# Kernel optimization log

Hardware: AMD Instinct MI355X
Metric: run time of the kernel (lower is better)

## Reference

```python
import jax, jax.numpy as jnp
import numpy as np
from functools import partial

B, N, T_HIST, T_FCST, HID, F, DEG = 16, 2000, 24, 24, 64, 8, 32
E_TOTAL = B * N * DEG


def setup_inputs() -> dict:
    key = jax.random.key(0)
    ks = jax.random.split(key, 20)
    s = 1.0 / np.sqrt(HID)
    # block-diagonal batched edge_index, as built by _process_adj_mat
    src = jax.random.randint(ks[0], (B, N * DEG), 0, N, dtype=jnp.int32)
    dst = jax.random.randint(ks[1], (B, N * DEG), 0, N, dtype=jnp.int32)
    off = (jnp.arange(B, dtype=jnp.int32) * N)[:, None]
    edge_index = jnp.stack([(src + off).reshape(-1), (dst + off).reshape(-1)], axis=0)
    return {
        "pm25_hist": jax.random.normal(ks[2], (B, T_HIST, N, 1), jnp.float32),
        "feature": jax.random.normal(ks[3], (B, T_HIST + T_FCST, N, F), jnp.float32),
        "edge_index": edge_index,
        "w_ih_enc": jax.random.normal(ks[4], (3 * HID, 2), jnp.float32) * s,
        "w_hh_enc": jax.random.normal(ks[5], (3 * HID, HID), jnp.float32) * s,
        "b_ih_enc": jnp.zeros((3 * HID,), jnp.float32),
        "b_hh_enc": jnp.zeros((3 * HID,), jnp.float32),
        "fc_w": jax.random.normal(ks[6], (1, HID), jnp.float32) * s,
        "fc_b": jnp.zeros((1,), jnp.float32),
        "cheb_w0": jax.random.normal(ks[7], (F + 1, 1), jnp.float32) * s,
        "cheb_w1": jax.random.normal(ks[8], (F + 1, 1), jnp.float32) * s,
        "cheb_b": jnp.zeros((1,), jnp.float32),
        "w_ih_dec": jax.random.normal(ks[9], (3 * HID, F + 2), jnp.float32) * s,
        "w_hh_dec": jax.random.normal(ks[10], (3 * HID, HID), jnp.float32) * s,
        "b_ih_dec": jnp.zeros((3 * HID,), jnp.float32),
        "b_hh_dec": jnp.zeros((3 * HID,), jnp.float32),
        "out_w": jax.random.normal(ks[11], (1, 2 * HID), jnp.float32) * s,
        "out_b": jnp.zeros((1,), jnp.float32),
    }


def gru(x, h, w_ih, w_hh, b_ih, b_hh):
    gi = x @ w_ih.T + b_ih
    gh = h @ w_hh.T + b_hh
    i_r, i_z, i_n = jnp.split(gi, 3, axis=-1)
    h_r, h_z, h_n = jnp.split(gh, 3, axis=-1)
    r = jax.nn.sigmoid(i_r + h_r)
    z = jax.nn.sigmoid(i_z + h_z)
    n = jnp.tanh(i_n + r * h_n)
    return (1.0 - z) * n + z * h


def cheb_conv(x, edge_index, w0, w1, b):
    # ChebConv K=2, sym norm, lambda_max=2 -> T1(L_hat) = -D^-1/2 A D^-1/2
    src, dst = edge_index[0], edge_index[1]
    ones = jnp.ones(src.shape, x.dtype)
    deg = jax.ops.segment_sum(ones, dst, num_segments=B * N)
    dis = jnp.where(deg > 0, jax.lax.rsqrt(jnp.maximum(deg, 1.0)), 0.0)
    norm = -(dis[src] * dis[dst])
    tx1 = jax.ops.segment_sum(norm[:, None] * x[src], dst, num_segments=B * N)
    return x @ w0 + tx1 @ w1 + b


def reference(pm25_hist, feature, edge_index, w_ih_enc, w_hh_enc, b_ih_enc, b_hh_enc,
              fc_w, fc_b, cheb_w0, cheb_w1, cheb_b, w_ih_dec, w_hh_dec, b_ih_dec,
              b_hh_dec, out_w, out_b):
    # ---------------- encoder ----------------
    h0 = jnp.zeros((B * N, HID), pm25_hist.dtype)
    x0 = jnp.zeros((B, N, 1), pm25_hist.dtype)

    def enc_step(carry, pm_t):
        hn, xn = carry
        x = jnp.concatenate([xn, pm_t], axis=-1).reshape(B * N, 2)
        hn = gru(x, hn, w_ih_enc, w_hh_enc, b_ih_enc, b_hh_enc)
        h3 = hn.reshape(B, N, HID)
        xn = h3 @ fc_w.T + fc_b
        return (hn, xn), h3

    (hn, xn), Hs = jax.lax.scan(enc_step, (h0, x0), pm25_hist.transpose(1, 0, 2, 3))
    H = Hs.transpose(1, 0, 2, 3)  # (B, T_HIST, N, HID)

    # ---------------- decoder ----------------
    def dec_step(carry, feat_t):
        hn, xn = carry
        x = jnp.concatenate([xn, feat_t], axis=-1)  # (B, N, F+1)
        xg = jax.nn.sigmoid(cheb_conv(x.reshape(B * N, F + 1), edge_index,
                                      cheb_w0, cheb_w1, cheb_b))
        x2 = jnp.concatenate([x, xg.reshape(B, N, 1)], axis=-1).reshape(B * N, F + 2)
        hn = gru(x2, hn, w_ih_dec, w_hh_dec, b_ih_dec, b_hh_dec)
        xn3 = hn.reshape(B, N, HID)
        energy = jnp.einsum('btnd,bnd->bnt', H, xn3)  # history attention
        alpha = jax.nn.softmax(energy, axis=2)
        a = jnp.einsum('bnt,btnd->bnd', alpha, H)
        xn = jnp.concatenate([a, xn3], axis=-1) @ out_w.T + out_b
        return (hn, xn), xn

    feats = feature[:, T_HIST:].transpose(1, 0, 2, 3)  # (T_FCST, B, N, F)
    _, preds = jax.lax.scan(dec_step, (hn, xn), feats)
    return preds.transpose(1, 0, 2, 3)  # (B, T_FCST, N, 1)
```

## Files before the change

### kernel.cpp

```cpp
#include <hip/hip_runtime.h>
#include <hip/hip_bf16.h>
#include <cstddef>
#include <cstdint>

constexpr int NB    = 16;
constexpr int NN    = 2000;
constexpr int TH    = 24;
constexpr int TF    = 24;
constexpr int HID   = 64;
constexpr int NF    = 8;
constexpr int NODES = NB * NN;
constexpr int ETOT  = NODES * 32;
constexpr int TT    = TH + TF;
constexpr int EBLK  = 32;
constexpr int NEBLK = NODES / EBLK;
constexpr int DBLK  = 64;
constexpr int NDBLK = NODES / DBLK;

typedef __attribute__((ext_vector_type(8))) short bf16x8;
typedef __attribute__((ext_vector_type(4))) float f32x4;
typedef uint16_t u16;

__device__ __forceinline__ float sigmoidf_(float x) { return 1.f / (1.f + __expf(-x)); }
__device__ __forceinline__ float tanhf_(float x) {
    float e = __expf(2.f * x);
    return 1.f - 2.f / (e + 1.f);
}
__device__ __forceinline__ u16 bfh(float x) {
    __hip_bfloat16 b = __float2bfloat16(x);
    u16 u; __builtin_memcpy(&u, &b, 2); return u;
}
__device__ __forceinline__ float bff(u16 u) { return __uint_as_float(((uint32_t)u) << 16); }
__device__ __forceinline__ uint32_t pk(u16 a, u16 b) { return (uint32_t)a | ((uint32_t)b << 16); }

__global__ void k_init(float* __restrict__ dis) {
    int i = blockIdx.x * blockDim.x + threadIdx.x;
    if (i < NODES) dis[i] = 0.f;
}

__global__ void k_deg(const int* __restrict__ ei, float* __restrict__ deg) {
    int e = blockIdx.x * blockDim.x + threadIdx.x;
    if (e < ETOT) atomicAdd(&deg[ei[ETOT + e]], 1.0f);
}

__global__ __launch_bounds__(256) void k_scan(const float* __restrict__ degf,
                                              int* __restrict__ row0,
                                              int* __restrict__ cnt)
{
    __shared__ int part[256];
    const int tid = threadIdx.x;
    const int per = NODES / 256;
    const int base = tid * per;
    int s = 0;
    for (int i = 0; i < per; i++) s += (int)degf[base + i];
    part[tid] = s;
    __syncthreads();
    for (int off = 1; off < 256; off <<= 1) {
        int v = (tid >= off) ? part[tid - off] : 0;
        __syncthreads();
        part[tid] += v;
        __syncthreads();
    }
    int run = (tid == 0) ? 0 : part[tid - 1];
    for (int i = 0; i < per; i++) {
        row0[base + i] = run;
        cnt[base + i]  = 0;
        run += (int)degf[base + i];
    }
    if (tid == 255) row0[NODES] = run;
}

__global__ void k_dis(float* __restrict__ dis) {
    int i = blockIdx.x * blockDim.x + threadIdx.x;
    if (i < NODES) {
        float d = dis[i];
        dis[i] = (d > 0.f) ? rsqrtf(fmaxf(d, 1.f)) : 0.f;
    }
}

__global__ void k_fill(const int* __restrict__ ei, const float* __restrict__ dis,
                       const int* __restrict__ row0, int* __restrict__ cnt,
                       int2* __restrict__ edge8)
{
    int e = blockIdx.x * blockDim.x + threadIdx.x;
    if (e < ETOT) {
        int s = ei[e];
        int d = ei[ETOT + e];
        float nv = -(dis[s] * dis[d]);
        int p = atomicAdd(&cnt[d], 1);
        edge8[row0[d] + p] = make_int2(s, __float_as_int(nv));
    }
}

__global__ void k_prepE(const float* __restrict__ whe, const float* __restrict__ fcw,
                        u16* __restrict__ AH, u16* __restrict__ AL)
{
    int i = blockIdx.x * blockDim.x + threadIdx.x;
    if (i < 208 * 64) {
        int r = i >> 6, k = i & 63;
        float v = (r < 192) ? whe[r * 64 + k] : ((r == 192) ? fcw[k] : 0.f);
        u16 hi = bfh(v);
        AH[i] = hi;
        AL[i] = bfh(v - bff(hi));
    }
}

__global__ void k_prepD(const float* __restrict__ whd, const float* __restrict__ wihd,
                        u16* __restrict__ AH, u16* __restrict__ AL)
{
    int i = blockIdx.x * blockDim.x + threadIdx.x;
    if (i < 256 * 96) {
        int r = i / 96, k = i - r * 96;
        float v = 0.f;
        if (k < 64) {
            if (r < 192) v = whd[r * 64 + k];
        } else if (k < 74) {
            int xi = k - 64;
            if (r < 128)       v = wihd[r * 10 + xi];
            else if (r >= 192) v = wihd[(r - 64) * 10 + xi];
        }
        u16 hi = bfh(v);
        AH[i] = hi;
        AL[i] = bfh(v - bff(hi));
    }
}

__global__ __launch_bounds__(256, 2) void k_encM(
    const float* __restrict__ pm, const u16* __restrict__ AeH, const u16* __restrict__ AeL,
    const float* __restrict__ w_ih, const float* __restrict__ b_ih, const float* __restrict__ b_hh,
    const float* __restrict__ fc_b, const float* __restrict__ feat, const float* __restrict__ cw1,
    u16* __restrict__ BgH, u16* __restrict__ BgL, u16* __restrict__ Hb,
    float* __restrict__ xn_buf, float* __restrict__ y1)
{
    __shared__ u16 BH[2][EBLK * 64], BL[2][EBLK * 64];
    __shared__ float pmL[TH * EBLK];
    __shared__ float xnL[EBLK];

    const int tid = threadIdx.x;
    const int l   = tid & 63;
    const int wv  = __builtin_amdgcn_readfirstlane(tid >> 6);
    const int n0  = blockIdx.x * EBLK;
    const int cn  = l & 15;
    const int kg  = l >> 4;
    const int c0  = wv * 16 + kg * 4;

    for (int i = tid; i < EBLK * 64 / 2; i += 256) {
        ((uint32_t*)BH[0])[i] = 0u;
        ((uint32_t*)BL[0])[i] = 0u;
    }
    for (int i = tid; i < TH * EBLK; i += 256) {
        int t = i >> 5, n = i & 31;
        int node = n0 + n, b = node / NN, nn2 = node - b * NN;
        pmL[i] = pm[(b * TH + t) * NN + nn2];
    }
    bf16x8 AHf[4][2], ALf[4][2];
    #pragma unroll
    for (int s = 0; s < 4; s++) {
        #pragma unroll
        for (int ks = 0; ks < 2; ks++) {
            bf16x8 zh = {0,0,0,0,0,0,0,0};
            AHf[s][ks] = zh; ALf[s][ks] = zh;
            if (s < 3 || wv == 0) {
                int row = (wv + 4 * s) * 16 + cn;
                int off = row * 64 + ks * 32 + kg * 8;
                AHf[s][ks] = *(const bf16x8*)(AeH + off);
                ALf[s][ks] = *(const bf16x8*)(AeL + off);
            }
        }
    }
    float bR[4], bZ[4], biN[4], bhN[4];
    float wR0[4], wR1[4], wZ0[4], wZ1[4], wN0[4], wN1[4];
    #pragma unroll
    for (int j = 0; j < 4; j++) {
        int c = c0 + j;
        bR[j]  = b_ih[c] + b_hh[c];
        bZ[j]  = b_ih[64 + c] + b_hh[64 + c];
        biN[j] = b_ih[128 + c];
        bhN[j] = b_hh[128 + c];
        wR0[j] = w_ih[2 * c];           wR1[j] = w_ih[2 * c + 1];
        wZ0[j] = w_ih[2 * (64 + c)];    wZ1[j] = w_ih[2 * (64 + c) + 1];
        wN0[j] = w_ih[2 * (128 + c)];   wN1[j] = w_ih[2 * (128 + c) + 1];
    }
    const float fcb = fc_b[0];
    int baddr[2][2], haddr[2];
    #pragma unroll
    for (int ct = 0; ct < 2; ct++) {
        const int n = ct * 16 + cn;
        #pragma unroll
        for (int ks = 0; ks < 2; ks++)
            baddr[ct][ks] = (n * 64 + ks * 32 + kg * 8) ^ ((n & 7) << 3);
        haddr[ct] = (n * 64 + c0) ^ ((n & 7) << 3);
    }
    const int xn_  = tid >> 3, xsl = tid & 7;
    const int xidx = (xn_ * 64 + xsl * 8) ^ ((xn_ & 7) << 3);
    u16* const xdst = Hb + (size_t)(n0 + xn_) * (TH * HID) + xsl * 8;
    float hreg[2][4] = {{0.f,0.f,0.f,0.f},{0.f,0.f,0.f,0.f}};
    __syncthreads();

    for (int t = 0; t < TH; t++) {
        const int cur = t & 1, nxt = cur ^ 1;
        f32x4 acc[4][2];
        #pragma unroll
        for (int s = 0; s < 4; s++)
            #pragma unroll
            for (int ct = 0; ct < 2; ct++)
                acc[s][ct] = (f32x4){0.f, 0.f, 0.f, 0.f};

        #pragma unroll
        for (int ct = 0; ct < 2; ct++) {
            #pragma unroll
            for (int ks = 0; ks < 2; ks++) {
                bf16x8 bh = *(const bf16x8*)&BH[cur][baddr[ct][ks]];
                bf16x8 bl = *(const bf16x8*)&BL[cur][baddr[ct][ks]];
                #pragma unroll
                for (int s = 0; s < 4; s++) {
                    if (s < 3 || wv == 0) {
                        acc[s][ct] = __builtin_amdgcn_mfma_f32_16x16x32_bf16(AHf[s][ks], bh, acc[s][ct], 0, 0, 0);
                        acc[s][ct] = __builtin_amdgcn_mfma_f32_16x16x32_bf16(AHf[s][ks], bl, acc[s][ct], 0, 0, 0);
                        acc[s][ct] = __builtin_amdgcn_mfma_f32_16x16x32_bf16(ALf[s][ks], bh, acc[s][ct], 0, 0, 0);
                    }
                }
            }
        }
        if (wv == 0 && kg == 0) {
            #pragma unroll
            for (int ct = 0; ct < 2; ct++) xnL[ct * 16 + cn] = acc[3][ct][0];
        }
        __syncthreads();

        #pragma unroll
        for (int ct = 0; ct < 2; ct++) {
            float xn = 0.f;
            if (t > 0) xn = xnL[ct * 16 + cn] + fcb;
            const float pv = pmL[t * EBLK + ct * 16 + cn];
            float hnew[4];
            #pragma unroll
            for (int j = 0; j < 4; j++) {
                float r  = sigmoidf_(acc[0][ct][j] + bR[j] + wR0[j] * xn + wR1[j] * pv);
                float z  = sigmoidf_(acc[1][ct][j] + bZ[j] + wZ0[j] * xn + wZ1[j] * pv);
                float gi = biN[j] + wN0[j] * xn + wN1[j] * pv;
                float gh = acc[2][ct][j] + bhN[j];
                float nn_ = tanhf_(gi + r * gh);
                hnew[j] = (1.f - z) * nn_ + z * hreg[ct][j];
                hreg[ct][j] = hnew[j];
            }
            u16 nh0 = bfh(hnew[0]), nh1 = bfh(hnew[1]), nh2 = bfh(hnew[2]), nh3 = bfh(hnew[3]);
            u16 nl0 = bfh(hnew[0] - bff(nh0)), nl1 = bfh(hnew[1] - bff(nh1));
            u16 nl2 = bfh(hnew[2] - bff(nh2)), nl3 = bfh(hnew[3] - bff(nh3));
            *(uint2*)&BH[nxt][haddr[ct]] = make_uint2(pk(nh0, nh1), pk(nh2, nh3));
            *(uint2*)&BL[nxt][haddr[ct]] = make_uint2(pk(nl0, nl1), pk(nl2, nl3));
        }
        __syncthreads();

        *(uint4*)(xdst + t * HID) = *(const uint4*)&BH[nxt][xidx];
    }

    if (wv == 0) {
        f32x4 ax[2];
        #pragma unroll
        for (int ct = 0; ct < 2; ct++) ax[ct] = (f32x4){0.f, 0.f, 0.f, 0.f};
        #pragma unroll
        for (int ct = 0; ct < 2; ct++) {
            #pragma unroll
            for (int ks = 0; ks < 2; ks++) {
                bf16x8 bh = *(const bf16x8*)&BH[0][baddr[ct][ks]];
                bf16x8 bl = *(const bf16x8*)&BL[0][baddr[ct][ks]];
                ax[ct] = __builtin_amdgcn_mfma_f32_16x16x32_bf16(AHf[3][ks], bh, ax[ct], 0, 0, 0);
                ax[ct] = __builtin_amdgcn_mfma_f32_16x16x32_bf16(AHf[3][ks], bl, ax[ct], 0, 0, 0);
                ax[ct] = __builtin_amdgcn_mfma_f32_16x16x32_bf16(ALf[3][ks], bh, ax[ct], 0, 0, 0);
            }
        }
        if (kg == 0) {
            #pragma unroll
            for (int ct = 0; ct < 2; ct++) xnL[ct * 16 + cn] = ax[ct][0];
        }
    }
    __syncthreads();

    {
        *(uint4*)(BgH + ((size_t)(n0 + xn_)) * 64 + xsl * 8) = *(const uint4*)&BH[0][xidx];
        *(uint4*)(BgL + ((size_t)(n0 + xn_)) * 64 + xsl * 8) = *(const uint4*)&BL[0][xidx];
    }
    if (tid < EBLK) {
        int n = tid, node = n0 + n;
        float xv = xnL[n] + fcb;
        xn_buf[node] = xv;
        int b = node / NN, nn2 = node - b * NN;
        const float* fp = feat + ((size_t)(b * TT + TH) * NN + nn2) * NF;
        float yy = xv * cw1[0];
        #pragma unroll
        for (int q = 0; q < NF; q++) yy += fp[q] * cw1[1 + q];
        y1[node] = yy;
    }
}

__global__ __launch_bounds__(256, 2) void k_decG(
    const float* __restrict__ feat, const u16* __restrict__ AdH, const u16* __restrict__ AdL,
    const float* __restrict__ b_ih, const float* __restrict__ b_hh,
    const float* __restrict__ w0, const float* __restrict__ cb,
    const float* __restrict__ xn_buf, const float* __restrict__ y1,
    const int* __restrict__ row0, const int2* __restrict__ edge8,
    const u16* __restrict__ BgHin, const u16* __restrict__ BgLin,
    u16* __restrict__ BgHout, u16* __restrict__ BgLout, int t)
{
    __shared__ u16 XH[64 * 96], XL[64 * 96];
    __shared__ float gpart[4][DBLK];
    const int tid = threadIdx.x;
    const int l   = tid & 63;
    const int wv  = __builtin_amdgcn_readfirstlane(tid >> 6);
    const int n0  = blockIdx.x * DBLK;
    const int cn  = l & 15, kg = l >> 4;
    const int c0  = wv * 16 + kg * 4;

    {
        const int na = tid >> 2;
        const int q  = tid & 3;
        const int nd = n0 + na;
        const int beg = row0[nd], end = row0[nd + 1];
        float acc = 0.f;
        for (int i = beg + q; i < end; i += 4) {
            const int2 e = edge8[i];
            acc = fmaf(__int_as_float(e.y), y1[e.x], acc);
        }
        gpart[q][na] = acc;
    }
    for (int i = tid; i < 512; i += 256) {
        int n = i >> 3, sl = i & 7;
        int idx = (n * 96 + sl * 8) ^ ((n & 7) << 3);
        *(uint4*)&XH[idx] = *(const uint4*)(BgHin + ((size_t)(n0 + n)) * 64 + sl * 8);
        *(uint4*)&XL[idx] = *(const uint4*)(BgLin + ((size_t)(n0 + n)) * 64 + sl * 8);
    }
    bf16x8 AHf[4][3], ALf[4][3];
    #pragma unroll
    for (int s = 0; s < 4; s++) {
        #pragma unroll
        for (int ks = 0; ks < 3; ks++) {
            bf16x8 zh = {0,0,0,0,0,0,0,0};
            AHf[s][ks] = zh; ALf[s][ks] = zh;
            const bool live = (s < 2) || (s == 2 && ks < 2) || (s == 3 && ks == 2);
            if (live) {
                int row = (wv + 4 * s) * 16 + cn;
                int off = row * 96 + ks * 32 + kg * 8;
                AHf[s][ks] = *(const bf16x8*)(AdH + off);
                ALf[s][ks] = *(const bf16x8*)(AdL + off);
            }
        }
    }
    float bsR[4], bsZ[4], biN[4], bhN[4];
    #pragma unroll
    for (int j = 0; j < 4; j++) {
        int c = c0 + j;
        bsR[j] = b_ih[c] + b_hh[c];
        bsZ[j] = b_ih[64 + c] + b_hh[64 + c];
        biN[j] = b_ih[128 + c];
        bhN[j] = b_hh[128 + c];
    }
    __syncthreads();

    if (tid < DBLK) {
        int n = tid, node = n0 + n;
        int b = node / NN, nn2 = node - b * NN;
        float txv = gpart[0][n] + gpart[1][n] + gpart[2][n] + gpart[3][n];
        float x0 = xn_buf[node];
        const float* fp = feat + ((size_t)(b * TT + TH + t) * NN + nn2) * NF;
        float f0 = fp[0], f1 = fp[1], f2 = fp[2], f3 = fp[3];
        float f4 = fp[4], f5 = fp[5], f6 = fp[6], f7 = fp[7];
        float xw = x0 * w0[0];
        xw = fmaf(f0, w0[1], xw); xw = fmaf(f1, w0[2], xw);
        xw = fmaf(f2, w0[3], xw); xw = fmaf(f3, w0[4], xw);
        xw = fmaf(f4, w0[5], xw); xw = fmaf(f5, w0[6], xw);
        xw = fmaf(f6, w0[7], xw); xw = fmaf(f7, w0[8], xw);
        float xg = sigmoidf_(xw + txv + cb[0]);
        u16 h0 = bfh(x0), h1 = bfh(f0), h2 = bfh(f1), h3 = bfh(f2), h4 = bfh(f3);
        u16 h5 = bfh(f4), h6 = bfh(f5), h7 = bfh(f6), h8 = bfh(f7), h9 = bfh(xg);
        u16 l0 = bfh(x0 - bff(h0)), l1 = bfh(f0 - bff(h1)), l2 = bfh(f1 - bff(h2));
        u16 l3 = bfh(f2 - bff(h3)), l4 = bfh(f3 - bff(h4)), l5 = bfh(f4 - bff(h5));
        u16 l6 = bfh(f5 - bff(h6)), l7 = bfh(f6 - bff(h7)), l8 = bfh(f7 - bff(h8));
        u16 l9 = bfh(xg - bff(h9));
        uint4 qh0 = make_uint4(pk(h0, h1), pk(h2, h3), pk(h4, h5), pk(h6, h7));
        uint4 qh1 = make_uint4(pk(h8, h9), 0u, 0u, 0u);
        uint4 ql0 = make_uint4(pk(l0, l1), pk(l2, l3), pk(l4, l5), pk(l6, l7));
        uint4 ql1 = make_uint4(pk(l8, l9), 0u, 0u, 0u);
        uint4 zz  = make_uint4(0u, 0u, 0u, 0u);
        const int sw = (n & 7) << 3;
        *(uint4*)&XH[(n * 96 + 64) ^ sw] = qh0;
        *(uint4*)&XH[(n * 96 + 72) ^ sw] = qh1;
        *(uint4*)&XH[(n * 96 + 80) ^ sw] = zz;
        *(uint4*)&XH[(n * 96 + 88) ^ sw] = zz;
        *(uint4*)&XL[(n * 96 + 64) ^ sw] = ql0;
        *(uint4*)&XL[(n * 96 + 72) ^ sw] = ql1;
        *(uint4*)&XL[(n * 96 + 80) ^ sw] = zz;
        *(uint4*)&XL[(n * 96 + 88) ^ sw] = zz;
    }
    __syncthreads();

    f32x4 acc[4][4];
    #pragma unroll
    for (int s = 0; s < 4; s++)
        #pragma unroll
        for (int ct = 0; ct < 4; ct++)
            acc[s][ct] = (f32x4){0.f, 0.f, 0.f, 0.f};

    #pragma unroll
    for (int ct = 0; ct < 4; ct++) {
        const int n = ct * 16 + cn;
        #pragma unroll
        for (int ks = 0; ks < 3; ks++) {
            const int idx = (n * 96 + ks * 32 + kg * 8) ^ ((n & 7) << 3);
            bf16x8 bh = *(const bf16x8*)&XH[idx];
            bf16x8 bl = *(const bf16x8*)&XL[idx];
            #pragma unroll
            for (int s = 0; s < 4; s++) {
                const bool live = (s < 2) || (s == 2 && ks < 2) || (s == 3 && ks == 2);
                if (live) {
                    acc[s][ct] = __builtin_amdgcn_mfma_f32_16x16x32_bf16(AHf[s][ks], bh, acc[s][ct], 0, 0, 0);
                    acc[s][ct] = __builtin_amdgcn_mfma_f32_16x16x32_bf16(AHf[s][ks], bl, acc[s][ct], 0, 0, 0);
                    acc[s][ct] = __builtin_amdgcn_mfma_f32_16x16x32_bf16(ALf[s][ks], bh, acc[s][ct], 0, 0, 0);
                }
            }
        }
    }

    #pragma unroll
    for (int ct = 0; ct < 4; ct++) {
        const int n = ct * 16 + cn, node = n0 + n;
        const int hidx = (n * 96 + c0) ^ ((n & 7) << 3);
        uint2 oh = *(const uint2*)&XH[hidx];
        uint2 ol = *(const uint2*)&XL[hidx];
        float hnew[4];
        #pragma unroll
        for (int j = 0; j < 4; j++) {
            u16 hh = (j < 2) ? (u16)((j == 0) ? (oh.x & 0xffff) : (oh.x >> 16))
                             : (u16)((j == 2) ? (oh.y & 0xffff) : (oh.y >> 16));
            u16 ll = (j < 2) ? (u16)((j == 0) ? (ol.x & 0xffff) : (ol.x >> 16))
                             : (u16)((j == 2) ? (ol.y & 0xffff) : (ol.y >> 16));
            float hold = bff(hh) + bff(ll);
            float r  = sigmoidf_(acc[0][ct][j] + bsR[j]);
            float z  = sigmoidf_(acc[1][ct][j] + bsZ[j]);
            float nn_ = tanhf_((acc[3][ct][j] + biN[j]) + r * (acc[2][ct][j] + bhN[j]));
            hnew[j] = (1.f - z) * nn_ + z * hold;
        }
        u16 nh0 = bfh(hnew[0]), nh1 = bfh(hnew[1]), nh2 = bfh(hnew[2]), nh3 = bfh(hnew[3]);
        u16 nl0 = bfh(hnew[0] - bff(nh0)), nl1 = bfh(hnew[1] - bff(nh1));
        u16 nl2 = bfh(hnew[2] - bff(nh2)), nl3 = bfh(hnew[3] - bff(nh3));
        *(uint2*)(BgHout + (size_t)node * 64 + c0) = make_uint2(pk(nh0, nh1), pk(nh2, nh3));
        *(uint2*)(BgLout + (size_t)node * 64 + c0) = make_uint2(pk(nl0, nl1), pk(nl2, nl3));
    }
}

__global__ __launch_bounds__(256) void k_attn(
    const u16* __restrict__ Hb, const u16* __restrict__ BgH, const u16* __restrict__ BgL,
    const float* __restrict__ out_w, const float* __restrict__ out_b,
    const float* __restrict__ feat, const float* __restrict__ cw1,
    float* __restrict__ xn_buf, float* __restrict__ y1,
    float* __restrict__ out, int t)
{
    const int wid  = threadIdx.x >> 6;
    const int lane = threadIdx.x & 63;
    const int node = blockIdx.x * 4 + wid;
    if (node >= NODES) return;
    const int d0 = (lane & 7) * 8;

    const float hj = bff(BgH[(size_t)node * 64 + lane]) + bff(BgL[(size_t)node * 64 + lane]);
    float hval[8];
    #pragma unroll
    for (int q = 0; q < 8; q++) hval[q] = __shfl(hj, d0 + q, 64);

    const uint4* Hrow = (const uint4*)(Hb + (size_t)node * (TH * HID));
    float Hf[3][8];
    float er[3];
    #pragma unroll
    for (int R = 0; R < 3; R++) {
        const uint4 v = Hrow[R * 64 + lane];
        const uint32_t u0 = v.x, u1 = v.y, u2 = v.z, u3 = v.w;
        Hf[R][0] = __uint_as_float(u0 << 16);
        Hf[R][1] = __uint_as_float(u0 & 0xffff0000u);
        Hf[R][2] = __uint_as_float(u1 << 16);
        Hf[R][3] = __uint_as_float(u1 & 0xffff0000u);
        Hf[R][4] = __uint_as_float(u2 << 16);
        Hf[R][5] = __uint_as_float(u2 & 0xffff0000u);
        Hf[R][6] = __uint_as_float(u3 << 16);
        Hf[R][7] = __uint_as_float(u3 & 0xffff0000u);
        float part = 0.f;
        #pragma unroll
        for (int q = 0; q < 8; q++) part = fmaf(Hf[R][q], hval[q], part);
        part += __shfl_xor(part, 1, 64);
        part += __shfl_xor(part, 2, 64);
        part += __shfl_xor(part, 4, 64);
        er[R] = part;
    }

    float m = fmaxf(fmaxf(er[0], er[1]), er[2]);
    m = fmaxf(m, __shfl_xor(m, 8, 64));
    m = fmaxf(m, __shfl_xor(m, 16, 64));
    m = fmaxf(m, __shfl_xor(m, 32, 64));

    float w0_ = __expf(er[0] - m);
    float w1_ = __expf(er[1] - m);
    float w2_ = __expf(er[2] - m);
    float s = w0_ + w1_ + w2_;
    s += __shfl_xor(s, 8, 64);
    s += __shfl_xor(s, 16, 64);
    s += __shfl_xor(s, 32, 64);
    const float rs = 1.f / s;

    float aq[8];
    #pragma unroll
    for (int q = 0; q < 8; q++) {
        float a = w0_ * Hf[0][q];
        a = fmaf(w1_, Hf[1][q], a);
        a = fmaf(w2_, Hf[2][q], a);
        a += __shfl_xor(a, 8, 64);
        a += __shfl_xor(a, 16, 64);
        a += __shfl_xor(a, 32, 64);
        aq[q] = a * rs;
    }

    float part = 0.f;
    #pragma unroll
    for (int q = 0; q < 8; q++) {
        part = fmaf(out_w[d0 + q],       aq[q],   part);
        part = fmaf(out_w[HID + d0 + q], hval[q], part);
    }
    part += __shfl_xor(part, 1, 64);
    part += __shfl_xor(part, 2, 64);
    part += __shfl_xor(part, 4, 64);
    const float xnew = part + out_b[0];

    if (lane == 0) {
        const int b = node / NN, n = node - b * NN;
        out[(b * TF + t) * NN + n] = xnew;
        xn_buf[node] = xnew;
        if (t + 1 < TF) {
            const float* fp = feat + ((size_t)(b * TT + TH + t + 1) * NN + n) * NF;
            float yy = xnew * cw1[0];
            #pragma unroll
            for (int c = 0; c < NF; c++) yy += fp[c] * cw1[1 + c];
            y1[node] = yy;
        }
    }
}

extern "C" void kernel_launch(void* const* d_in, const int* in_sizes, int n_in,
                              void* d_out, int out_size, void* d_ws, size_t ws_size,
                              hipStream_t stream)
{
    const float* pm     = (const float*)d_in[0];
    const float* feat   = (const float*)d_in[1];
    const int*   ei     = (const int*)d_in[2];
    const float* w_ih_e = (const float*)d_in[3];
    const float* w_hh_e = (const float*)d_in[4];
    const float* b_ih_e = (const float*)d_in[5];
    const float* b_hh_e = (const float*)d_in[6];
    const float* fc_w   = (const float*)d_in[7];
    const float* fc_b   = (const float*)d_in[8];
    const float* cw0    = (const float*)d_in[9];
    const float* cw1    = (const float*)d_in[10];
    const float* cb     = (const float*)d_in[11];
    const float* w_ih_d = (const float*)d_in[12];
    const float* w_hh_d = (const float*)d_in[13];
    const float* b_ih_d = (const float*)d_in[14];
    const float* b_hh_d = (const float*)d_in[15];
    const float* out_w  = (const float*)d_in[16];
    const float* out_b  = (const float*)d_in[17];
    float* out = (float*)d_out;

    char* ws = (char*)d_ws;
    size_t off = 0;
    auto alloc = [&](size_t bytes) -> void* {
        void* p = ws + off;
        off += (bytes + 255) & ~(size_t)255;
        return p;
    };
    u16* Hb    = (u16*)alloc(sizeof(u16) * (size_t)NODES * TH * HID);
    u16* BgAH  = (u16*)alloc(sizeof(u16) * (size_t)NODES * HID);
    u16* BgAL  = (u16*)alloc(sizeof(u16) * (size_t)NODES * HID);
    u16* BgBH  = (u16*)alloc(sizeof(u16) * (size_t)NODES * HID);
    u16* BgBL  = (u16*)alloc(sizeof(u16) * (size_t)NODES * HID);
    float* xn  = (float*)alloc(sizeof(float) * NODES);
    float* dis = (float*)alloc(sizeof(float) * NODES);
    float* y1  = (float*)alloc(sizeof(float) * NODES);
    u16* AeH   = (u16*)alloc(sizeof(u16) * 208 * 64);
    u16* AeL   = (u16*)alloc(sizeof(u16) * 208 * 64);
    u16* AdH   = (u16*)alloc(sizeof(u16) * 256 * 96);
    u16* AdL   = (u16*)alloc(sizeof(u16) * 256 * 96);
    int* row0  = (int*)alloc(sizeof(int) * (NODES + 1));
    int* cnt   = (int*)alloc(sizeof(int) * NODES);
    int2* edge8 = (int2*)alloc(sizeof(int2) * ETOT);
    if (off > ws_size) return;

    k_init<<<(NODES + 255) / 256, 256, 0, stream>>>(dis);
    k_deg<<<(ETOT + 255) / 256, 256, 0, stream>>>(ei, dis);
    k_scan<<<1, 256, 0, stream>>>(dis, row0, cnt);
    k_dis<<<(NODES + 255) / 256, 256, 0, stream>>>(dis);
    k_fill<<<(ETOT + 255) / 256, 256, 0, stream>>>(ei, dis, row0, cnt, edge8);
    k_prepE<<<(208 * 64 + 255) / 256, 256, 0, stream>>>(w_hh_e, fc_w, AeH, AeL);
    k_prepD<<<(256 * 96 + 255) / 256, 256, 0, stream>>>(w_hh_d, w_ih_d, AdH, AdL);

    k_encM<<<NEBLK, 256, 0, stream>>>(pm, AeH, AeL, w_ih_e, b_ih_e, b_hh_e,
                                      fc_b, feat, cw1, BgAH, BgAL, Hb, xn, y1);

    for (int t = 0; t < TF; t++) {
        const u16* inH = (t & 1) ? BgBH : BgAH;
        const u16* inL = (t & 1) ? BgBL : BgAL;
        u16* outH      = (t & 1) ? BgAH : BgBH;
        u16* outL      = (t & 1) ? BgAL : BgBL;
        k_decG<<<NDBLK, 256, 0, stream>>>(feat, AdH, AdL, b_ih_d, b_hh_d,
                                          cw0, cb, xn, y1, row0, edge8,
                                          inH, inL, outH, outL, t);
        k_attn<<<NODES / 4, 256, 0, stream>>>(Hb, outH, outL, out_w, out_b, feat, cw1,
                                              xn, y1, out, t);
    }
}
```

Baseline: 1.147 ms.

## Fuse decoder attention into GRU kernel with online softmax over history

```diff
diff --git a/kernel.cpp b/kernel.cpp
--- a/kernel.cpp
+++ b/kernel.cpp
@@ -294,17 +294,20 @@
     }
 }
 
-__global__ __launch_bounds__(256, 2) void k_decG(
+__global__ __launch_bounds__(256, 2) void k_decA(
     const float* __restrict__ feat, const u16* __restrict__ AdH, const u16* __restrict__ AdL,
     const float* __restrict__ b_ih, const float* __restrict__ b_hh,
     const float* __restrict__ w0, const float* __restrict__ cb,
-    const float* __restrict__ xn_buf, const float* __restrict__ y1,
+    float* __restrict__ xn_buf, const float* __restrict__ y1_in, float* __restrict__ y1_out,
     const int* __restrict__ row0, const int2* __restrict__ edge8,
-    const u16* __restrict__ BgHin, const u16* __restrict__ BgLin,
-    u16* __restrict__ BgHout, u16* __restrict__ BgLout, int t)
+    u16* __restrict__ BgH, u16* __restrict__ BgL,
+    const u16* __restrict__ Hb, const float* __restrict__ out_w, const float* __restrict__ out_b,
+    const float* __restrict__ cw1, float* __restrict__ out, int t)
 {
     __shared__ u16 XH[64 * 96], XL[64 * 96];
     __shared__ float gpart[4][DBLK];
+    __shared__ float hx[DBLK][68];
+
     const int tid = threadIdx.x;
     const int l   = tid & 63;
     const int wv  = __builtin_amdgcn_readfirstlane(tid >> 6);
@@ -320,15 +323,15 @@
         float acc = 0.f;
         for (int i = beg + q; i < end; i += 4) {
             const int2 e = edge8[i];
-            acc = fmaf(__int_as_float(e.y), y1[e.x], acc);
+            acc = fmaf(__int_as_float(e.y), y1_in[e.x], acc);
         }
         gpart[q][na] = acc;
     }
     for (int i = tid; i < 512; i += 256) {
         int n = i >> 3, sl = i & 7;
         int idx = (n * 96 + sl * 8) ^ ((n & 7) << 3);
-        *(uint4*)&XH[idx] = *(const uint4*)(BgHin + ((size_t)(n0 + n)) * 64 + sl * 8);
-        *(uint4*)&XL[idx] = *(const uint4*)(BgLin + ((size_t)(n0 + n)) * 64 + sl * 8);
+        *(uint4*)&XH[idx] = *(const uint4*)(BgH + ((size_t)(n0 + n)) * 64 + sl * 8);
+        *(uint4*)&XL[idx] = *(const uint4*)(BgL + ((size_t)(n0 + n)) * 64 + sl * 8);
     }
     bf16x8 AHf[4][3], ALf[4][3];
     #pragma unroll
@@ -443,100 +446,78 @@
         u16 nh0 = bfh(hnew[0]), nh1 = bfh(hnew[1]), nh2 = bfh(hnew[2]), nh3 = bfh(hnew[3]);
         u16 nl0 = bfh(hnew[0] - bff(nh0)), nl1 = bfh(hnew[1] - bff(nh1));
         u16 nl2 = bfh(hnew[2] - bff(nh2)), nl3 = bfh(hnew[3] - bff(nh3));
-        *(uint2*)(BgHout + (size_t)node * 64 + c0) = make_uint2(pk(nh0, nh1), pk(nh2, nh3));
-        *(uint2*)(BgLout + (size_t)node * 64 + c0) = make_uint2(pk(nl0, nl1), pk(nl2, nl3));
-    }
-}
-
-__global__ __launch_bounds__(256) void k_attn(
-    const u16* __restrict__ Hb, const u16* __restrict__ BgH, const u16* __restrict__ BgL,
-    const float* __restrict__ out_w, const float* __restrict__ out_b,
-    const float* __restrict__ feat, const float* __restrict__ cw1,
-    float* __restrict__ xn_buf, float* __restrict__ y1,
-    float* __restrict__ out, int t)
-{
-    const int wid  = threadIdx.x >> 6;
-    const int lane = threadIdx.x & 63;
-    const int node = blockIdx.x * 4 + wid;
-    if (node >= NODES) return;
-    const int d0 = (lane & 7) * 8;
-
-    const float hj = bff(BgH[(size_t)node * 64 + lane]) + bff(BgL[(size_t)node * 64 + lane]);
-    float hval[8];
-    #pragma unroll
-    for (int q = 0; q < 8; q++) hval[q] = __shfl(hj, d0 + q, 64);
-
-    const uint4* Hrow = (const uint4*)(Hb + (size_t)node * (TH * HID));
-    float Hf[3][8];
-    float er[3];
-    #pragma unroll
-    for (int R = 0; R < 3; R++) {
-        const uint4 v = Hrow[R * 64 + lane];
-        const uint32_t u0 = v.x, u1 = v.y, u2 = v.z, u3 = v.w;
-        Hf[R][0] = __uint_as_float(u0 << 16);
-        Hf[R][1] = __uint_as_float(u0 & 0xffff0000u);
-        Hf[R][2] = __uint_as_float(u1 << 16);
-        Hf[R][3] = __uint_as_float(u1 & 0xffff0000u);
-        Hf[R][4] = __uint_as_float(u2 << 16);
-        Hf[R][5] = __uint_as_float(u2 & 0xffff0000u);
-        Hf[R][6] = __uint_as_float(u3 << 16);
-        Hf[R][7] = __uint_as_float(u3 & 0xffff0000u);
+        *(uint2*)(BgH + (size_t)node * 64 + c0) = make_uint2(pk(nh0, nh1), pk(nh2, nh3));
+        *(uint2*)(BgL + (size_t)node * 64 + c0) = make_uint2(pk(nl0, nl1), pk(nl2, nl3));
+        *(float4*)&hx[n][c0] = make_float4(hnew[0], hnew[1], hnew[2], hnew[3]);
+    }
+    __syncthreads();
+
+    {
+        const int g = tid >> 2;
+        const int q = tid & 3;
+        const int node = n0 + g;
+        float hval[16];
+        #pragma unroll
+        for (int i = 0; i < 4; i++) {
+            float4 v = *(const float4*)&hx[g][q * 16 + 4 * i];
+            hval[4 * i]     = v.x; hval[4 * i + 1] = v.y;
+            hval[4 * i + 2] = v.z; hval[4 * i + 3] = v.w;
+        }
+        const u16* Hrow = Hb + (size_t)node * (TH * HID) + q * 16;
+
+        float m = -3.0e38f, s = 0.f;
+        float aq[16];
+        #pragma unroll
+        for (int i = 0; i < 16; i++) aq[i] = 0.f;
+
+        for (int tt = 0; tt < TH; tt++) {
+            const uint4 v0 = *(const uint4*)(Hrow + tt * HID);
+            const uint4 v1 = *(const uint4*)(Hrow + tt * HID + 8);
+            float Hf[16];
+            Hf[0]  = __uint_as_float(v0.x << 16); Hf[1]  = __uint_as_float(v0.x & 0xffff0000u);
+            Hf[2]  = __uint_as_float(v0.y << 16); Hf[3]  = __uint_as_float(v0.y & 0xffff0000u);
+            Hf[4]  = __uint_as_float(v0.z << 16); Hf[5]  = __uint_as_float(v0.z & 0xffff0000u);
+            Hf[6]  = __uint_as_float(v0.w << 16); Hf[7]  = __uint_as_float(v0.w & 0xffff0000u);
+            Hf[8]  = __uint_as_float(v1.x << 16); Hf[9]  = __uint_as_float(v1.x & 0xffff0000u);
+            Hf[10] = __uint_as_float(v1.y << 16); Hf[11] = __uint_as_float(v1.y & 0xffff0000u);
+            Hf[12] = __uint_as_float(v1.z << 16); Hf[13] = __uint_as_float(v1.z & 0xffff0000u);
+            Hf[14] = __uint_as_float(v1.w << 16); Hf[15] = __uint_as_float(v1.w & 0xffff0000u);
+            float p = 0.f;
+            #pragma unroll
+            for (int i = 0; i < 16; i++) p = fmaf(Hf[i], hval[i], p);
+            p += __shfl_xor(p, 1, 64);
+            p += __shfl_xor(p, 2, 64);
+            const float mn = fmaxf(m, p);
+            const float c  = __expf(m - mn);
+            const float w  = __expf(p - mn);
+            s = s * c + w;
+            #pragma unroll
+            for (int i = 0; i < 16; i++) aq[i] = fmaf(aq[i], c, w * Hf[i]);
+            m = mn;
+        }
+        const float rs = 1.f / s;
+
         float part = 0.f;
         #pragma unroll
-        for (int q = 0; q < 8; q++) part = fmaf(Hf[R][q], hval[q], part);
+        for (int i = 0; i < 16; i++) {
+            part = fmaf(out_w[q * 16 + i],       aq[i] * rs, part);
+            part = fmaf(out_w[HID + q * 16 + i], hval[i],    part);
+        }
         part += __shfl_xor(part, 1, 64);
         part += __shfl_xor(part, 2, 64);
-        part += __shfl_xor(part, 4, 64);
-        er[R] = part;
-    }
-
-    float m = fmaxf(fmaxf(er[0], er[1]), er[2]);
-    m = fmaxf(m, __shfl_xor(m, 8, 64));
-    m = fmaxf(m, __shfl_xor(m, 16, 64));
-    m = fmaxf(m, __shfl_xor(m, 32, 64));
-
-    float w0_ = __expf(er[0] - m);
-    float w1_ = __expf(er[1] - m);
-    float w2_ = __expf(er[2] - m);
-    float s = w0_ + w1_ + w2_;
-    s += __shfl_xor(s, 8, 64);
-    s += __shfl_xor(s, 16, 64);
-    s += __shfl_xor(s, 32, 64);
-    const float rs = 1.f / s;
-
-    float aq[8];
-    #pragma unroll
-    for (int q = 0; q < 8; q++) {
-        float a = w0_ * Hf[0][q];
-        a = fmaf(w1_, Hf[1][q], a);
-        a = fmaf(w2_, Hf[2][q], a);
-        a += __shfl_xor(a, 8, 64);
-        a += __shfl_xor(a, 16, 64);
-        a += __shfl_xor(a, 32, 64);
-        aq[q] = a * rs;
-    }
-
-    float part = 0.f;
-    #pragma unroll
-    for (int q = 0; q < 8; q++) {
-        part = fmaf(out_w[d0 + q],       aq[q],   part);
-        part = fmaf(out_w[HID + d0 + q], hval[q], part);
-    }
-    part += __shfl_xor(part, 1, 64);
-    part += __shfl_xor(part, 2, 64);
-    part += __shfl_xor(part, 4, 64);
-    const float xnew = part + out_b[0];
-
-    if (lane == 0) {
-        const int b = node / NN, n = node - b * NN;
-        out[(b * TF + t) * NN + n] = xnew;
-        xn_buf[node] = xnew;
-        if (t + 1 < TF) {
-            const float* fp = feat + ((size_t)(b * TT + TH + t + 1) * NN + n) * NF;
-            float yy = xnew * cw1[0];
-            #pragma unroll
-            for (int c = 0; c < NF; c++) yy += fp[c] * cw1[1 + c];
-            y1[node] = yy;
+        const float xnew = part + out_b[0];
+
+        if (q == 0) {
+            const int b = node / NN, n = node - b * NN;
+            out[(b * TF + t) * NN + n] = xnew;
+            xn_buf[node] = xnew;
+            if (t + 1 < TF) {
+                const float* fp = feat + ((size_t)(b * TT + TH + t + 1) * NN + n) * NF;
+                float yy = xnew * cw1[0];
+                #pragma unroll
+                for (int c2 = 0; c2 < NF; c2++) yy += fp[c2] * cw1[1 + c2];
+                y1_out[node] = yy;
+            }
         }
     }
 }
@@ -573,13 +554,12 @@
         return p;
     };
     u16* Hb    = (u16*)alloc(sizeof(u16) * (size_t)NODES * TH * HID);
-    u16* BgAH  = (u16*)alloc(sizeof(u16) * (size_t)NODES * HID);
-    u16* BgAL  = (u16*)alloc(sizeof(u16) * (size_t)NODES * HID);
-    u16* BgBH  = (u16*)alloc(sizeof(u16) * (size_t)NODES * HID);
-    u16* BgBL  = (u16*)alloc(sizeof(u16) * (size_t)NODES * HID);
+    u16* BgH   = (u16*)alloc(sizeof(u16) * (size_t)NODES * HID);
+    u16* BgL   = (u16*)alloc(sizeof(u16) * (size_t)NODES * HID);
     float* xn  = (float*)alloc(sizeof(float) * NODES);
     float* dis = (float*)alloc(sizeof(float) * NODES);
-    float* y1  = (float*)alloc(sizeof(float) * NODES);
+    float* y1A = (float*)alloc(sizeof(float) * NODES);
+    float* y1B = (float*)alloc(sizeof(float) * NODES);
     u16* AeH   = (u16*)alloc(sizeof(u16) * 208 * 64);
     u16* AeL   = (u16*)alloc(sizeof(u16) * 208 * 64);
     u16* AdH   = (u16*)alloc(sizeof(u16) * 256 * 96);
@@ -598,17 +578,13 @@
     k_prepD<<<(256 * 96 + 255) / 256, 256, 0, stream>>>(w_hh_d, w_ih_d, AdH, AdL);
 
     k_encM<<<NEBLK, 256, 0, stream>>>(pm, AeH, AeL, w_ih_e, b_ih_e, b_hh_e,
-                                      fc_b, feat, cw1, BgAH, BgAL, Hb, xn, y1);
+                                      fc_b, feat, cw1, BgH, BgL, Hb, xn, y1A);
 
     for (int t = 0; t < TF; t++) {
-        const u16* inH = (t & 1) ? BgBH : BgAH;
-        const u16* inL = (t & 1) ? BgBL : BgAL;
-        u16* outH      = (t & 1) ? BgAH : BgBH;
-        u16* outL      = (t & 1) ? BgAL : BgBL;
-        k_decG<<<NDBLK, 256, 0, stream>>>(feat, AdH, AdL, b_ih_d, b_hh_d,
-                                          cw0, cb, xn, y1, row0, edge8,
-                                          inH, inL, outH, outL, t);
-        k_attn<<<NODES / 4, 256, 0, stream>>>(Hb, outH, outL, out_w, out_b, feat, cw1,
-                                              xn, y1, out, t);
-    }
-}
+        const float* yin = (t & 1) ? y1B : y1A;
+        float* yout      = (t & 1) ? y1A : y1B;
+        k_decA<<<NDBLK, 256, 0, stream>>>(feat, AdH, AdL, b_ih_d, b_hh_d,
+                                          cw0, cb, xn, yin, yout, row0, edge8,
+                                          BgH, BgL, Hb, out_w, out_b, cw1, out, t);
+    }
+}
```

Measured after the change: 1.012 ms, median of 3. 11.8% less time.
